# Kernel tuning notes

Hardware: AMD Instinct MI355X
Metric: run time of the kernel (lower is better)

## Reference

```python
import jax, jax.numpy as jnp
import numpy as np

B, T, D = 4, 8192, 1024
BLOCKS, TOPK, MACRO, SLOTS = 64, 16, 4, 64
RMS_EPS = 1.1920929e-07  # torch.finfo(float32).eps, F.rms_norm default


def setup_inputs() -> dict:
    key = jax.random.key(0)
    ks = jax.random.split(key, 7)
    return {
        "prev_hidden": jax.random.normal(ks[0], (B, T, D), jnp.float32),
        "prev_nll": jax.random.uniform(ks[1], (B, T), jnp.float32),
        "query": jax.random.normal(ks[2], (SLOTS, D), jnp.float32) * 0.02,
        "W_sum": jax.random.normal(ks[3], (D, 2 * D), jnp.float32) / np.sqrt(2 * D),
        "W_k": jax.random.normal(ks[4], (D, D), jnp.float32) / np.sqrt(D),
        "W_v": jax.random.normal(ks[5], (D, D), jnp.float32) / np.sqrt(D),
        "W_o": jax.random.normal(ks[6], (D, D), jnp.float32) / np.sqrt(D),
    }


def _rms_norm(x):
    return x * jax.lax.rsqrt(jnp.mean(x * x, axis=-1, keepdims=True) + RMS_EPS)


def _zscore(x):
    m = x.mean(axis=1, keepdims=True)
    s = jnp.maximum(x.std(axis=1, keepdims=True), 1e-6)  # unbiased=False
    return (x - m) / s


def reference(prev_hidden, prev_nll, query, W_sum, W_k, W_v, W_o):
    b, t, d = prev_hidden.shape
    # --- micro segments: equal blocks (t divisible by BLOCKS -> linspace edges exact)
    L = t // BLOCKS
    seg = prev_hidden.reshape(b, BLOCKS, L, d)
    seg_mean = seg.mean(axis=2)          # [B, BLOCKS, D]
    seg_last = seg[:, :, -1, :]          # [B, BLOCKS, D]
    hid_score = jnp.linalg.norm(seg_mean, axis=-1)            # [B, BLOCKS]
    sur_score = prev_nll.reshape(b, BLOCKS, L).mean(axis=-1)  # [B, BLOCKS]
    scores = _zscore(hid_score) + _zscore(sur_score)          # utility_source='both'
    idx = jnp.sort(jax.lax.top_k(scores, TOPK)[1], axis=-1)   # [B, TOPK]
    gmean = jnp.take_along_axis(seg_mean, idx[:, :, None], axis=1)
    glast = jnp.take_along_axis(seg_last, idx[:, :, None], axis=1)
    micro = jnp.concatenate([gmean, glast], axis=-1)          # [B, TOPK, 2D]
    # --- hierarchical: macro segments + global
    Lm = t // MACRO
    mseg = prev_hidden.reshape(b, MACRO, Lm, d)
    macro = jnp.concatenate([mseg.mean(axis=2), mseg[:, :, -1, :]], axis=-1)
    glob = jnp.concatenate([prev_hidden.mean(axis=1), prev_hidden[:, -1, :]], axis=-1)[:, None, :]
    feats = jnp.concatenate([micro, macro, glob], axis=1)     # [B, S=21, 2D]
    summaries = _rms_norm(jnp.einsum('bsf,df->bsd', feats, W_sum))
    # --- cross-attention of learned prefix queries over sources
    keys = jnp.einsum('bsd,ed->bse', summaries, W_k)
    vals = jnp.einsum('bsd,ed->bse', summaries, W_v)
    logits = jnp.einsum('qd,bsd->bqs', query, keys) / jnp.sqrt(jnp.float32(d))
    attn = jax.nn.softmax(logits.astype(jnp.float32), axis=-1).astype(summaries.dtype)
    prefix = jnp.einsum('bqs,bse->bqe', attn, vals)
    return jnp.einsum('bqe,oe->bqo', prefix, W_o)
```

## Files before the change

### kernel.cpp

```cpp
#include <hip/hip_runtime.h>
#include <stdint.h>
#include <stddef.h>

#define B_ 4
#define T_ 8192
#define D_ 1024
#define NBLK 64
#define SEGL 128
#define TOPK_ 16
#define NS 21
#define MPAD 96
#define RMS_EPS_ 1.1920929e-07f
#define PART 98304

typedef float f32x4 __attribute__((ext_vector_type(4)));
typedef __bf16 bf16x8 __attribute__((ext_vector_type(8)));
typedef unsigned short us8 __attribute__((ext_vector_type(8)));

__device__ __forceinline__ unsigned short f2bf(float f) {
    union { float f; unsigned int u; } v; v.f = f;
    unsigned int r = v.u + 0x7FFFu + ((v.u >> 16) & 1u);
    return (unsigned short)(r >> 16);
}
__device__ __forceinline__ float4 ld4(const float* p) { return *(const float4*)p; }

__global__ __launch_bounds__(1024) void seg_stats(
        const float* __restrict__ ph, const float* __restrict__ nll,
        float* __restrict__ seg_mean, float* __restrict__ hid, float* __restrict__ sur) {
    int g = blockIdx.x; int b = g >> 6; int blk = g & 63;
    int tid = threadIdx.x; int chunk = tid >> 8; int c = tid & 255;
    const float* base = ph + ((size_t)b * T_ + blk * SEGL + chunk * 32) * D_ + 4 * c;
    const float* p0 = base;
    const float* p1 = base + (size_t)8  * D_;
    const float* p2 = base + (size_t)16 * D_;
    const float* p3 = base + (size_t)24 * D_;
    f32x4 a0 = {0,0,0,0}, a1 = {0,0,0,0}, a2 = {0,0,0,0}, a3 = {0,0,0,0};
    #pragma unroll
    for (int r = 0; r < 8; r++) {
        float4 v0 = ld4(p0 + (size_t)r * D_);
        float4 v1 = ld4(p1 + (size_t)r * D_);
        float4 v2 = ld4(p2 + (size_t)r * D_);
        float4 v3 = ld4(p3 + (size_t)r * D_);
        a0.x += v0.x; a0.y += v0.y; a0.z += v0.z; a0.w += v0.w;
        a1.x += v1.x; a1.y += v1.y; a1.z += v1.z; a1.w += v1.w;
        a2.x += v2.x; a2.y += v2.y; a2.z += v2.z; a2.w += v2.w;
        a3.x += v3.x; a3.y += v3.y; a3.z += v3.z; a3.w += v3.w;
    }
    float sx = a0.x + a1.x + a2.x + a3.x;
    float sy = a0.y + a1.y + a2.y + a3.y;
    float sz = a0.z + a1.z + a2.z + a3.z;
    float sw = a0.w + a1.w + a2.w + a3.w;

    __shared__ float4 tmp[3][256];
    __shared__ float redw[4];
    __shared__ float surw;
    if (chunk) {
        float4 t; t.x = sx; t.y = sy; t.z = sz; t.w = sw;
        tmp[chunk - 1][c] = t;
        if (tid >= 256 && tid < 320) {
            int i = tid - 256;
            float v = nll[b * T_ + blk * SEGL + i] + nll[b * T_ + blk * SEGL + 64 + i];
            #pragma unroll
            for (int o = 32; o; o >>= 1) v += __shfl_xor(v, o);
            if (i == 0) surw = v * (1.f/128.f);
        }
    }
    __syncthreads();
    if (chunk == 0) {
        float4 t0 = tmp[0][c], t1 = tmp[1][c], t2 = tmp[2][c];
        float mx = (sx + t0.x + t1.x + t2.x) * (1.f/128.f);
        float my = (sy + t0.y + t1.y + t2.y) * (1.f/128.f);
        float mz = (sz + t0.z + t1.z + t2.z) * (1.f/128.f);
        float mw = (sw + t0.w + t1.w + t2.w) * (1.f/128.f);
        float4 m; m.x = mx; m.y = my; m.z = mz; m.w = mw;
        *(float4*)(seg_mean + (size_t)g * D_ + 4 * c) = m;
        float rv = mx*mx + my*my + mz*mz + mw*mw;
        #pragma unroll
        for (int o = 32; o; o >>= 1) rv += __shfl_xor(rv, o);
        if ((tid & 63) == 0) redw[tid >> 6] = rv;
    }
    __syncthreads();
    if (tid == 0) {
        hid[g] = sqrtf(redw[0] + redw[1] + redw[2] + redw[3]);
        sur[g] = surw;
    }
}

__global__ __launch_bounds__(256) void feats_build(
        const float* __restrict__ ph, const float* __restrict__ seg_mean,
        const float* __restrict__ hid, const float* __restrict__ sur,
        unsigned short* __restrict__ feats) {
    int r = blockIdx.x; int t = threadIdx.x;
    unsigned short* row0 = feats + (size_t)r * 2048 + 4 * t;
    unsigned short* row1 = row0 + 1024;
    if (r >= B_ * NS) {
        ushort4 z4; z4.x = z4.y = z4.z = z4.w = 0;
        *(ushort4*)row0 = z4; *(ushort4*)row1 = z4;
        return;
    }
    int b = r / NS, s = r % NS;
    __shared__ float sc[64];
    __shared__ int sidx[16];
    if (t < 64) {
        float h = hid[b * NBLK + t];
        float ss0 = sur[b * NBLK + t];
        float mh = h; for (int o = 32; o; o >>= 1) mh += __shfl_xor(mh, o); mh *= (1.f/64.f);
        float dh = h - mh; float vh = dh * dh;
        for (int o = 32; o; o >>= 1) vh += __shfl_xor(vh, o); vh *= (1.f/64.f);
        float sh = fmaxf(sqrtf(vh), 1e-6f);
        float ms = ss0; for (int o = 32; o; o >>= 1) ms += __shfl_xor(ms, o); ms *= (1.f/64.f);
        float ds = ss0 - ms; float vs = ds * ds;
        for (int o = 32; o; o >>= 1) vs += __shfl_xor(vs, o); vs *= (1.f/64.f);
        float ssd = fmaxf(sqrtf(vs), 1e-6f);
        sc[t] = dh / sh + ds / ssd;
    }
    __syncthreads();
    if (t < 64) {
        float z = sc[t];
        int rank = 0;
        for (int j = 0; j < 64; j++) {
            float oj = sc[j];
            rank += (oj > z) || (oj == z && j < t);
        }
        bool sel = rank < TOPK_;
        unsigned long long mask = __ballot(sel);
        int pos = __popcll(mask & ((1ull << t) - 1ull));
        if (sel) sidx[pos] = t;
    }
    __syncthreads();

    float mx = 0, my = 0, mz = 0, mw = 0;
    int lastrow;
    if (s < 16) {
        int blk = sidx[s];
        float4 v = ld4(seg_mean + (size_t)(b * NBLK + blk) * D_ + 4 * t);
        mx = v.x; my = v.y; mz = v.z; mw = v.w;
        lastrow = blk * SEGL + SEGL - 1;
    } else if (s < 20) {
        int m = s - 16;
        for (int j = 0; j < 16; j++) {
            float4 v = ld4(seg_mean + (size_t)(b * NBLK + m * 16 + j) * D_ + 4 * t);
            mx += v.x; my += v.y; mz += v.z; mw += v.w;
        }
        mx *= (1.f/16.f); my *= (1.f/16.f); mz *= (1.f/16.f); mw *= (1.f/16.f);
        lastrow = m * 2048 + 2047;
    } else {
        for (int j = 0; j < 64; j++) {
            float4 v = ld4(seg_mean + (size_t)(b * NBLK + j) * D_ + 4 * t);
            mx += v.x; my += v.y; mz += v.z; mw += v.w;
        }
        mx *= (1.f/64.f); my *= (1.f/64.f); mz *= (1.f/64.f); mw *= (1.f/64.f);
        lastrow = T_ - 1;
    }
    float4 lv = ld4(ph + ((size_t)b * T_ + lastrow) * D_ + 4 * t);
    ushort4 hm; hm.x = f2bf(mx); hm.y = f2bf(my); hm.z = f2bf(mz); hm.w = f2bf(mw);
    ushort4 hl; hl.x = f2bf(lv.x); hl.y = f2bf(lv.y); hl.z = f2bf(lv.z); hl.w = f2bf(lv.w);
    *(ushort4*)row0 = hm;
    *(ushort4*)row1 = hl;
}

template<int K, int AMODE, int FULLK>
__global__ __launch_bounds__(512) void gemm_lds(
        const void* __restrict__ Av,
        const float* __restrict__ B0, const float* __restrict__ B1,
        float* __restrict__ C0, float* __restrict__ C1) {
    const float* Bw = blockIdx.z ? B1 : B0;
    float* Cp       = blockIdx.z ? C1 : C0;
    int n0 = blockIdx.x * 64;
    if (!FULLK) Cp += (size_t)blockIdx.y * PART;
    int tid = threadIdx.x, wave = tid >> 6, lane = tid & 63;
    int quad = lane >> 4, l16 = lane & 15;

    __shared__ __align__(16) unsigned short Bs[64 * 264];
    __shared__ __align__(16) unsigned short As[96 * 264];

    int strip = wave >> 1, kh = wave & 1;
    f32x4 acc[6];
    #pragma unroll
    for (int i = 0; i < 6; i++) acc[i] = (f32x4){0.f, 0.f, 0.f, 0.f};
    const unsigned short* bbase = &Bs[(strip * 16 + l16) * 264 + kh * 128 + quad * 8];
    const unsigned short* abase = &As[l16 * 264 + kh * 128 + quad * 8];

    const int NCH = FULLK ? (K / 256) : 1;
    for (int ci = 0; ci < NCH; ci++) {
        int kc = FULLK ? ci : (int)blockIdx.y;
        if (ci) __syncthreads();
        #pragma unroll
        for (int i = 0; i < 4; i++) {
            int id = tid + 512 * i;
            int r = id >> 5, c = id & 31;
            const float* src = Bw + (size_t)(n0 + r) * K + kc * 256 + c * 8;
            float4 v0 = ld4(src), v1 = ld4(src + 4);
            us8 h;
            h[0] = f2bf(v0.x); h[1] = f2bf(v0.y); h[2] = f2bf(v0.z); h[3] = f2bf(v0.w);
            h[4] = f2bf(v1.x); h[5] = f2bf(v1.y); h[6] = f2bf(v1.z); h[7] = f2bf(v1.w);
            *(us8*)&Bs[r * 264 + c * 8] = h;
        }
        #pragma unroll
        for (int i = 0; i < 6; i++) {
            int id = tid + 512 * i;
            int r = id >> 5, c = id & 31;
            if (AMODE == 0) {
                const unsigned short* A = (const unsigned short*)Av;
                *(us8*)&As[r * 264 + c * 8] =
                    *(const us8*)(A + (size_t)r * K + kc * 256 + c * 8);
            } else {
                const float* A = (const float*)Av;
                const float* s0 = A + (size_t)r * K + kc * 256 + c * 8;
                float4 a0 = ld4(s0), a1 = ld4(s0 + 4);
                us8 h;
                h[0] = f2bf(a0.x); h[1] = f2bf(a0.y); h[2] = f2bf(a0.z); h[3] = f2bf(a0.w);
                h[4] = f2bf(a1.x); h[5] = f2bf(a1.y); h[6] = f2bf(a1.z); h[7] = f2bf(a1.w);
                *(us8*)&As[r * 264 + c * 8] = h;
            }
        }
        __syncthreads();
        #pragma unroll
        for (int kk = 0; kk < 128; kk += 32) {
            bf16x8 bfr = __builtin_bit_cast(bf16x8, *(const us8*)(bbase + kk));
            #pragma unroll
            for (int mi = 0; mi < 6; mi++) {
                bf16x8 af = __builtin_bit_cast(bf16x8, *(const us8*)(abase + mi * 16 * 264 + kk));
                acc[mi] = __builtin_amdgcn_mfma_f32_16x16x32_bf16(af, bfr, acc[mi], 0, 0, 0);
            }
        }
    }
    __syncthreads();

    float* scr = (float*)As;
    const int SS = 68;
    if (kh == 1) {
        #pragma unroll
        for (int mi = 0; mi < 6; mi++)
            #pragma unroll
            for (int r = 0; r < 4; r++)
                scr[(mi * 16 + quad * 4 + r) * SS + strip * 16 + l16] = acc[mi][r];
    }
    __syncthreads();
    if (kh == 0) {
        #pragma unroll
        for (int mi = 0; mi < 6; mi++)
            #pragma unroll
            for (int r = 0; r < 4; r++)
                scr[(mi * 16 + quad * 4 + r) * SS + strip * 16 + l16] += acc[mi][r];
    }
    __syncthreads();
    #pragma unroll
    for (int i = 0; i < 3; i++) {
        int id = tid + 512 * i;
        int row = id >> 4, c4 = (id & 15) << 2;
        float4 v = *(const float4*)&scr[row * SS + c4];
        *(float4*)&Cp[(size_t)row * 1024 + n0 + c4] = v;
    }
}

__global__ __launch_bounds__(256) void rmsnorm8(
        const float* __restrict__ pp, unsigned short* __restrict__ y) {
    int r = blockIdx.x; int t = threadIdx.x;
    float4 v = (float4){0.f, 0.f, 0.f, 0.f};
    #pragma unroll
    for (int c = 0; c < 8; c++) {
        float4 u = ld4(pp + (size_t)c * PART + (size_t)r * D_ + 4 * t);
        v.x += u.x; v.y += u.y; v.z += u.z; v.w += u.w;
    }
    __shared__ float red[256];
    red[t] = v.x*v.x + v.y*v.y + v.z*v.z + v.w*v.w;
    __syncthreads();
    for (int s2 = 128; s2 > 0; s2 >>= 1) { if (t < s2) red[t] += red[t + s2]; __syncthreads(); }
    float scale = rsqrtf(red[0] * (1.f/1024.f) + RMS_EPS_);
    ushort4 h;
    h.x = f2bf(v.x * scale); h.y = f2bf(v.y * scale);
    h.z = f2bf(v.z * scale); h.w = f2bf(v.w * scale);
    *(ushort4*)(y + (size_t)r * D_ + 4 * t) = h;
}

__global__ __launch_bounds__(256) void attn_out(
        const float* __restrict__ query, const float* __restrict__ keys,
        const float* __restrict__ valsO, float* __restrict__ out) {
    int g = blockIdx.x; int b = g >> 6; int q = g & 63;
    int tid = threadIdx.x, wave = tid >> 6, lane = tid & 63;
    __shared__ float attnw[24];
    const float* qrow = query + (size_t)q * D_ + lane * 16;
    float4 qv0 = ld4(qrow), qv1 = ld4(qrow + 4), qv2 = ld4(qrow + 8), qv3 = ld4(qrow + 12);
    for (int s = wave; s < NS; s += 4) {
        const float* kp = keys + (size_t)(b * NS + s) * D_ + lane * 16;
        float4 u0 = ld4(kp), u1 = ld4(kp + 4), u2 = ld4(kp + 8), u3 = ld4(kp + 12);
        float a = qv0.x*u0.x + qv0.y*u0.y + qv0.z*u0.z + qv0.w*u0.w
                + qv1.x*u1.x + qv1.y*u1.y + qv1.z*u1.z + qv1.w*u1.w
                + qv2.x*u2.x + qv2.y*u2.y + qv2.z*u2.z + qv2.w*u2.w
                + qv3.x*u3.x + qv3.y*u3.y + qv3.z*u3.z + qv3.w*u3.w;
        for (int o = 32; o; o >>= 1) a += __shfl_xor(a, o);
        if (lane == 0) attnw[s] = a * 0.03125f;
    }
    __syncthreads();
    if (tid < 32) {
        float v = (tid < NS) ? attnw[tid] : -3.0e38f;
        float m = v;
        #pragma unroll
        for (int o = 16; o; o >>= 1) m = fmaxf(m, __shfl_xor(m, o));
        float e = (tid < NS) ? expf(v - m) : 0.f;
        float s2 = e;
        #pragma unroll
        for (int o = 16; o; o >>= 1) s2 += __shfl_xor(s2, o);
        if (tid < NS) attnw[tid] = e / s2;
    }
    __syncthreads();
    float ax = 0, ay = 0, az = 0, aw = 0;
    #pragma unroll
    for (int s = 0; s < NS; s++) {
        float w = attnw[s];
        float4 v = ld4(valsO + (size_t)(b * NS + s) * D_ + 4 * tid);
        ax += w * v.x; ay += w * v.y; az += w * v.z; aw += w * v.w;
    }
    float4 o4; o4.x = ax; o4.y = ay; o4.z = az; o4.w = aw;
    *(float4*)(out + (size_t)g * D_ + 4 * tid) = o4;
}

extern "C" void kernel_launch(void* const* d_in, const int* in_sizes, int n_in,
                              void* d_out, int out_size, void* d_ws, size_t ws_size,
                              hipStream_t stream) {
    (void)in_sizes; (void)n_in; (void)out_size; (void)ws_size;
    const float* ph    = (const float*)d_in[0];
    const float* nll   = (const float*)d_in[1];
    const float* query = (const float*)d_in[2];
    const float* W_sum = (const float*)d_in[3];
    const float* W_k   = (const float*)d_in[4];
    const float* W_v   = (const float*)d_in[5];
    const float* W_o   = (const float*)d_in[6];
    float* out = (float*)d_out;

    char* ws = (char*)d_ws;
    float*          seg_mean = (float*)(ws + 0);
    float*          hid      = (float*)(ws + 1048576);
    float*          sur      = (float*)(ws + 1049600);
    unsigned short* feats    = (unsigned short*)(ws + 1050624);
    float*          presum_p = (float*)(ws + 1443840);
    unsigned short* summ_b   = (unsigned short*)(ws + 4589568);
    float*          keys     = (float*)(ws + 4786176);
    float*          vals     = (float*)(ws + 5179392);
    float*          valsO    = (float*)(ws + 5572608);

    seg_stats<<<B_ * NBLK, 1024, 0, stream>>>(ph, nll, seg_mean, hid, sur);
    feats_build<<<MPAD, 256, 0, stream>>>(ph, seg_mean, hid, sur, feats);
    gemm_lds<2048, 0, 0><<<dim3(16, 8, 1), 512, 0, stream>>>(
        feats, W_sum, nullptr, presum_p, nullptr);
    rmsnorm8<<<MPAD, 256, 0, stream>>>(presum_p, summ_b);
    gemm_lds<1024, 0, 1><<<dim3(16, 1, 2), 512, 0, stream>>>(
        summ_b, W_k, W_v, keys, vals);
    gemm_lds<1024, 2, 1><<<dim3(16, 1, 1), 512, 0, stream>>>(
        vals, W_o, nullptr, valsO, nullptr);
    attn_out<<<B_ * NBLK, 256, 0, stream>>>(query, keys, valsO, out);
}
```

Measured before the change: 260.0 us.

## Fuse post-stats pipeline into one cooperative persistent kernel with grid syncs

Six small launches (feats build, W_sum GEMM, rmsnorm, K/V GEMM, W_o GEMM, attention) are replaced by one cooperative 128-block kernel separated by grid.sync barriers. The K/V and W_o GEMMs are also split along K into partial-sum buffers that later stages reduce on load, which gives more blocks work in those phases. The aim is to remove launch gaps and raise parallelism in the GEMMs that previously ran on only 16–32 blocks. In exchange it pays grid-sync costs and redundant partial-sum reads, and it depends on cooperative launch residency.

Measured after the change: 460.7 us. 77.2% more time.

```diff
diff --git a/kernel.cpp b/kernel.cpp
--- a/kernel.cpp
+++ b/kernel.cpp
@@ -1,6 +1,9 @@
 #include <hip/hip_runtime.h>
+#include <hip/hip_cooperative_groups.h>
 #include <stdint.h>
 #include <stddef.h>
+
+namespace cg = cooperative_groups;
 
 #define B_ 4
 #define T_ 8192
@@ -86,143 +89,64 @@
     }
 }
 
-__global__ __launch_bounds__(256) void feats_build(
-        const float* __restrict__ ph, const float* __restrict__ seg_mean,
-        const float* __restrict__ hid, const float* __restrict__ sur,
-        unsigned short* __restrict__ feats) {
-    int r = blockIdx.x; int t = threadIdx.x;
-    unsigned short* row0 = feats + (size_t)r * 2048 + 4 * t;
-    unsigned short* row1 = row0 + 1024;
-    if (r >= B_ * NS) {
-        ushort4 z4; z4.x = z4.y = z4.z = z4.w = 0;
-        *(ushort4*)row0 = z4; *(ushort4*)row1 = z4;
-        return;
-    }
-    int b = r / NS, s = r % NS;
-    __shared__ float sc[64];
-    __shared__ int sidx[16];
-    if (t < 64) {
-        float h = hid[b * NBLK + t];
-        float ss0 = sur[b * NBLK + t];
-        float mh = h; for (int o = 32; o; o >>= 1) mh += __shfl_xor(mh, o); mh *= (1.f/64.f);
-        float dh = h - mh; float vh = dh * dh;
-        for (int o = 32; o; o >>= 1) vh += __shfl_xor(vh, o); vh *= (1.f/64.f);
-        float sh = fmaxf(sqrtf(vh), 1e-6f);
-        float ms = ss0; for (int o = 32; o; o >>= 1) ms += __shfl_xor(ms, o); ms *= (1.f/64.f);
-        float ds = ss0 - ms; float vs = ds * ds;
-        for (int o = 32; o; o >>= 1) vs += __shfl_xor(vs, o); vs *= (1.f/64.f);
-        float ssd = fmaxf(sqrtf(vs), 1e-6f);
-        sc[t] = dh / sh + ds / ssd;
-    }
-    __syncthreads();
-    if (t < 64) {
-        float z = sc[t];
-        int rank = 0;
-        for (int j = 0; j < 64; j++) {
-            float oj = sc[j];
-            rank += (oj > z) || (oj == z && j < t);
-        }
-        bool sel = rank < TOPK_;
-        unsigned long long mask = __ballot(sel);
-        int pos = __popcll(mask & ((1ull << t) - 1ull));
-        if (sel) sidx[pos] = t;
-    }
-    __syncthreads();
-
-    float mx = 0, my = 0, mz = 0, mw = 0;
-    int lastrow;
-    if (s < 16) {
-        int blk = sidx[s];
-        float4 v = ld4(seg_mean + (size_t)(b * NBLK + blk) * D_ + 4 * t);
-        mx = v.x; my = v.y; mz = v.z; mw = v.w;
-        lastrow = blk * SEGL + SEGL - 1;
-    } else if (s < 20) {
-        int m = s - 16;
-        for (int j = 0; j < 16; j++) {
-            float4 v = ld4(seg_mean + (size_t)(b * NBLK + m * 16 + j) * D_ + 4 * t);
-            mx += v.x; my += v.y; mz += v.z; mw += v.w;
-        }
-        mx *= (1.f/16.f); my *= (1.f/16.f); mz *= (1.f/16.f); mw *= (1.f/16.f);
-        lastrow = m * 2048 + 2047;
-    } else {
-        for (int j = 0; j < 64; j++) {
-            float4 v = ld4(seg_mean + (size_t)(b * NBLK + j) * D_ + 4 * t);
-            mx += v.x; my += v.y; mz += v.z; mw += v.w;
-        }
-        mx *= (1.f/64.f); my *= (1.f/64.f); mz *= (1.f/64.f); mw *= (1.f/64.f);
-        lastrow = T_ - 1;
-    }
-    float4 lv = ld4(ph + ((size_t)b * T_ + lastrow) * D_ + 4 * t);
-    ushort4 hm; hm.x = f2bf(mx); hm.y = f2bf(my); hm.z = f2bf(mz); hm.w = f2bf(mw);
-    ushort4 hl; hl.x = f2bf(lv.x); hl.y = f2bf(lv.y); hl.z = f2bf(lv.z); hl.w = f2bf(lv.w);
-    *(ushort4*)row0 = hm;
-    *(ushort4*)row1 = hl;
-}
-
-template<int K, int AMODE, int FULLK>
-__global__ __launch_bounds__(512) void gemm_lds(
-        const void* __restrict__ Av,
-        const float* __restrict__ B0, const float* __restrict__ B1,
-        float* __restrict__ C0, float* __restrict__ C1) {
-    const float* Bw = blockIdx.z ? B1 : B0;
-    float* Cp       = blockIdx.z ? C1 : C0;
-    int n0 = blockIdx.x * 64;
-    if (!FULLK) Cp += (size_t)blockIdx.y * PART;
-    int tid = threadIdx.x, wave = tid >> 6, lane = tid & 63;
+template<int K, int AMODE>
+__device__ __forceinline__ void gemm_chunk(
+        const void* __restrict__ Av, const float* __restrict__ Bw,
+        float* __restrict__ Cp, int n0, int kc, int tid,
+        unsigned short* Bs, unsigned short* As) {
+    int wave = tid >> 6, lane = tid & 63;
     int quad = lane >> 4, l16 = lane & 15;
-
-    __shared__ __align__(16) unsigned short Bs[64 * 264];
-    __shared__ __align__(16) unsigned short As[96 * 264];
-
     int strip = wave >> 1, kh = wave & 1;
+
+    #pragma unroll
+    for (int i = 0; i < 4; i++) {
+        int id = tid + 512 * i;
+        int r = id >> 5, c = id & 31;
+        const float* src = Bw + (size_t)(n0 + r) * K + kc * 256 + c * 8;
+        float4 v0 = ld4(src), v1 = ld4(src + 4);
+        us8 h;
+        h[0] = f2bf(v0.x); h[1] = f2bf(v0.y); h[2] = f2bf(v0.z); h[3] = f2bf(v0.w);
+        h[4] = f2bf(v1.x); h[5] = f2bf(v1.y); h[6] = f2bf(v1.z); h[7] = f2bf(v1.w);
+        *(us8*)&Bs[r * 264 + c * 8] = h;
+    }
+    #pragma unroll
+    for (int i = 0; i < 6; i++) {
+        int id = tid + 512 * i;
+        int r = id >> 5, c = id & 31;
+        if (AMODE == 0) {
+            const unsigned short* A = (const unsigned short*)Av;
+            *(us8*)&As[r * 264 + c * 8] =
+                *(const us8*)(A + (size_t)r * K + kc * 256 + c * 8);
+        } else {
+            const float* A = (const float*)Av;
+            const float* s0 = A + (size_t)r * 1024 + kc * 256 + c * 8;
+            float4 a0 = ld4(s0), a1 = ld4(s0 + 4);
+            #pragma unroll
+            for (int p = 1; p < 4; p++) {
+                float4 b0 = ld4(s0 + p * PART), b1 = ld4(s0 + p * PART + 4);
+                a0.x += b0.x; a0.y += b0.y; a0.z += b0.z; a0.w += b0.w;
+                a1.x += b1.x; a1.y += b1.y; a1.z += b1.z; a1.w += b1.w;
+            }
+            us8 h;
+            h[0] = f2bf(a0.x); h[1] = f2bf(a0.y); h[2] = f2bf(a0.z); h[3] = f2bf(a0.w);
+            h[4] = f2bf(a1.x); h[5] = f2bf(a1.y); h[6] = f2bf(a1.z); h[7] = f2bf(a1.w);
+            *(us8*)&As[r * 264 + c * 8] = h;
+        }
+    }
+    __syncthreads();
+
     f32x4 acc[6];
     #pragma unroll
     for (int i = 0; i < 6; i++) acc[i] = (f32x4){0.f, 0.f, 0.f, 0.f};
     const unsigned short* bbase = &Bs[(strip * 16 + l16) * 264 + kh * 128 + quad * 8];
     const unsigned short* abase = &As[l16 * 264 + kh * 128 + quad * 8];
-
-    const int NCH = FULLK ? (K / 256) : 1;
-    for (int ci = 0; ci < NCH; ci++) {
-        int kc = FULLK ? ci : (int)blockIdx.y;
-        if (ci) __syncthreads();
+    #pragma unroll
+    for (int kk = 0; kk < 128; kk += 32) {
+        bf16x8 bfr = __builtin_bit_cast(bf16x8, *(const us8*)(bbase + kk));
         #pragma unroll
-        for (int i = 0; i < 4; i++) {
-            int id = tid + 512 * i;
-            int r = id >> 5, c = id & 31;
-            const float* src = Bw + (size_t)(n0 + r) * K + kc * 256 + c * 8;
-            float4 v0 = ld4(src), v1 = ld4(src + 4);
-            us8 h;
-            h[0] = f2bf(v0.x); h[1] = f2bf(v0.y); h[2] = f2bf(v0.z); h[3] = f2bf(v0.w);
-            h[4] = f2bf(v1.x); h[5] = f2bf(v1.y); h[6] = f2bf(v1.z); h[7] = f2bf(v1.w);
-            *(us8*)&Bs[r * 264 + c * 8] = h;
-        }
-        #pragma unroll
-        for (int i = 0; i < 6; i++) {
-            int id = tid + 512 * i;
-            int r = id >> 5, c = id & 31;
-            if (AMODE == 0) {
-                const unsigned short* A = (const unsigned short*)Av;
-                *(us8*)&As[r * 264 + c * 8] =
-                    *(const us8*)(A + (size_t)r * K + kc * 256 + c * 8);
-            } else {
-                const float* A = (const float*)Av;
-                const float* s0 = A + (size_t)r * K + kc * 256 + c * 8;
-                float4 a0 = ld4(s0), a1 = ld4(s0 + 4);
-                us8 h;
-                h[0] = f2bf(a0.x); h[1] = f2bf(a0.y); h[2] = f2bf(a0.z); h[3] = f2bf(a0.w);
-                h[4] = f2bf(a1.x); h[5] = f2bf(a1.y); h[6] = f2bf(a1.z); h[7] = f2bf(a1.w);
-                *(us8*)&As[r * 264 + c * 8] = h;
-            }
-        }
-        __syncthreads();
-        #pragma unroll
-        for (int kk = 0; kk < 128; kk += 32) {
-            bf16x8 bfr = __builtin_bit_cast(bf16x8, *(const us8*)(bbase + kk));
-            #pragma unroll
-            for (int mi = 0; mi < 6; mi++) {
-                bf16x8 af = __builtin_bit_cast(bf16x8, *(const us8*)(abase + mi * 16 * 264 + kk));
-                acc[mi] = __builtin_amdgcn_mfma_f32_16x16x32_bf16(af, bfr, acc[mi], 0, 0, 0);
-            }
+        for (int mi = 0; mi < 6; mi++) {
+            bf16x8 af = __builtin_bit_cast(bf16x8, *(const us8*)(abase + mi * 16 * 264 + kk));
+            acc[mi] = __builtin_amdgcn_mfma_f32_16x16x32_bf16(af, bfr, acc[mi], 0, 0, 0);
         }
     }
     __syncthreads();
@@ -254,66 +178,200 @@
     }
 }
 
-__global__ __launch_bounds__(256) void rmsnorm8(
-        const float* __restrict__ pp, unsigned short* __restrict__ y) {
-    int r = blockIdx.x; int t = threadIdx.x;
-    float4 v = (float4){0.f, 0.f, 0.f, 0.f};
-    #pragma unroll
-    for (int c = 0; c < 8; c++) {
-        float4 u = ld4(pp + (size_t)c * PART + (size_t)r * D_ + 4 * t);
-        v.x += u.x; v.y += u.y; v.z += u.z; v.w += u.w;
-    }
-    __shared__ float red[256];
-    red[t] = v.x*v.x + v.y*v.y + v.z*v.z + v.w*v.w;
-    __syncthreads();
-    for (int s2 = 128; s2 > 0; s2 >>= 1) { if (t < s2) red[t] += red[t + s2]; __syncthreads(); }
-    float scale = rsqrtf(red[0] * (1.f/1024.f) + RMS_EPS_);
-    ushort4 h;
-    h.x = f2bf(v.x * scale); h.y = f2bf(v.y * scale);
-    h.z = f2bf(v.z * scale); h.w = f2bf(v.w * scale);
-    *(ushort4*)(y + (size_t)r * D_ + 4 * t) = h;
-}
-
-__global__ __launch_bounds__(256) void attn_out(
-        const float* __restrict__ query, const float* __restrict__ keys,
-        const float* __restrict__ valsO, float* __restrict__ out) {
-    int g = blockIdx.x; int b = g >> 6; int q = g & 63;
-    int tid = threadIdx.x, wave = tid >> 6, lane = tid & 63;
-    __shared__ float attnw[24];
-    const float* qrow = query + (size_t)q * D_ + lane * 16;
-    float4 qv0 = ld4(qrow), qv1 = ld4(qrow + 4), qv2 = ld4(qrow + 8), qv3 = ld4(qrow + 12);
-    for (int s = wave; s < NS; s += 4) {
-        const float* kp = keys + (size_t)(b * NS + s) * D_ + lane * 16;
-        float4 u0 = ld4(kp), u1 = ld4(kp + 4), u2 = ld4(kp + 8), u3 = ld4(kp + 12);
-        float a = qv0.x*u0.x + qv0.y*u0.y + qv0.z*u0.z + qv0.w*u0.w
-                + qv1.x*u1.x + qv1.y*u1.y + qv1.z*u1.z + qv1.w*u1.w
-                + qv2.x*u2.x + qv2.y*u2.y + qv2.z*u2.z + qv2.w*u2.w
-                + qv3.x*u3.x + qv3.y*u3.y + qv3.z*u3.z + qv3.w*u3.w;
-        for (int o = 32; o; o >>= 1) a += __shfl_xor(a, o);
-        if (lane == 0) attnw[s] = a * 0.03125f;
-    }
-    __syncthreads();
-    if (tid < 32) {
-        float v = (tid < NS) ? attnw[tid] : -3.0e38f;
-        float m = v;
+__global__ __launch_bounds__(512) void mega(
+        const float* __restrict__ ph, const float* __restrict__ query,
+        const float* __restrict__ W_sum, const float* __restrict__ W_k,
+        const float* __restrict__ W_v, const float* __restrict__ W_o,
+        const float* __restrict__ seg_mean, const float* __restrict__ hid,
+        const float* __restrict__ sur,
+        unsigned short* __restrict__ feats, float* __restrict__ presum_p,
+        unsigned short* __restrict__ summ_b,
+        float* __restrict__ keys_p, float* __restrict__ vals_p,
+        float* __restrict__ valsO_p, float* __restrict__ out) {
+    cg::grid_group grid = cg::this_grid();
+    __shared__ __align__(16) unsigned short smem_us[160 * 264];
+    unsigned short* Bs = smem_us;
+    unsigned short* As = smem_us + 64 * 264;
+    int bid = blockIdx.x, tid = threadIdx.x;
+
+    if (bid < MPAD) {
+        int r = bid, t = tid;
+        if (r >= B_ * NS) {
+            if (t < 256) {
+                ushort4 z4; z4.x = z4.y = z4.z = z4.w = 0;
+                unsigned short* row0 = feats + (size_t)r * 2048 + 4 * t;
+                *(ushort4*)row0 = z4; *(ushort4*)(row0 + 1024) = z4;
+            }
+        } else {
+            int b = r / NS, s = r % NS;
+            float* sc = (float*)smem_us;
+            int* sidx = (int*)(smem_us + 128);
+            if (t < 64) {
+                float h = hid[b * NBLK + t];
+                float ss0 = sur[b * NBLK + t];
+                float mh = h; for (int o = 32; o; o >>= 1) mh += __shfl_xor(mh, o); mh *= (1.f/64.f);
+                float dh = h - mh; float vh = dh * dh;
+                for (int o = 32; o; o >>= 1) vh += __shfl_xor(vh, o); vh *= (1.f/64.f);
+                float sh = fmaxf(sqrtf(vh), 1e-6f);
+                float ms = ss0; for (int o = 32; o; o >>= 1) ms += __shfl_xor(ms, o); ms *= (1.f/64.f);
+                float ds = ss0 - ms; float vs = ds * ds;
+                for (int o = 32; o; o >>= 1) vs += __shfl_xor(vs, o); vs *= (1.f/64.f);
+                float ssd = fmaxf(sqrtf(vs), 1e-6f);
+                sc[t] = dh / sh + ds / ssd;
+            }
+            __syncthreads();
+            if (t < 64) {
+                float z = sc[t];
+                int rank = 0;
+                for (int j = 0; j < 64; j++) {
+                    float oj = sc[j];
+                    rank += (oj > z) || (oj == z && j < t);
+                }
+                bool sel = rank < TOPK_;
+                unsigned long long mask = __ballot(sel);
+                int pos = __popcll(mask & ((1ull << t) - 1ull));
+                if (sel) sidx[pos] = t;
+            }
+            __syncthreads();
+            if (t < 256) {
+                float mx = 0, my = 0, mz = 0, mw = 0;
+                int lastrow;
+                if (s < 16) {
+                    int blk = sidx[s];
+                    float4 v = ld4(seg_mean + (size_t)(b * NBLK + blk) * D_ + 4 * t);
+                    mx = v.x; my = v.y; mz = v.z; mw = v.w;
+                    lastrow = blk * SEGL + SEGL - 1;
+                } else if (s < 20) {
+                    int m = s - 16;
+                    for (int j = 0; j < 16; j++) {
+                        float4 v = ld4(seg_mean + (size_t)(b * NBLK + m * 16 + j) * D_ + 4 * t);
+                        mx += v.x; my += v.y; mz += v.z; mw += v.w;
+                    }
+                    mx *= (1.f/16.f); my *= (1.f/16.f); mz *= (1.f/16.f); mw *= (1.f/16.f);
+                    lastrow = m * 2048 + 2047;
+                } else {
+                    for (int j = 0; j < 64; j++) {
+                        float4 v = ld4(seg_mean + (size_t)(b * NBLK + j) * D_ + 4 * t);
+                        mx += v.x; my += v.y; mz += v.z; mw += v.w;
+                    }
+                    mx *= (1.f/64.f); my *= (1.f/64.f); mz *= (1.f/64.f); mw *= (1.f/64.f);
+                    lastrow = T_ - 1;
+                }
+                float4 lv = ld4(ph + ((size_t)b * T_ + lastrow) * D_ + 4 * t);
+                ushort4 hm; hm.x = f2bf(mx); hm.y = f2bf(my); hm.z = f2bf(mz); hm.w = f2bf(mw);
+                ushort4 hl; hl.x = f2bf(lv.x); hl.y = f2bf(lv.y); hl.z = f2bf(lv.z); hl.w = f2bf(lv.w);
+                unsigned short* row0 = feats + (size_t)r * 2048 + 4 * t;
+                *(ushort4*)row0 = hm;
+                *(ushort4*)(row0 + 1024) = hl;
+            }
+        }
+    }
+    __threadfence(); grid.sync();
+
+    {
+        int strip = bid >> 3, kc = bid & 7;
+        gemm_chunk<2048, 0>(feats, W_sum, presum_p + (size_t)kc * PART,
+                            strip * 64, kc, tid, Bs, As);
+    }
+    __threadfence(); grid.sync();
+
+    if (bid < MPAD) {
+        int r = bid, t = tid;
+        float* red = (float*)smem_us;
+        float4 v = (float4){0.f, 0.f, 0.f, 0.f};
+        if (t < 256) {
+            #pragma unroll
+            for (int c = 0; c < 8; c++) {
+                float4 u = ld4(presum_p + (size_t)c * PART + (size_t)r * D_ + 4 * t);
+                v.x += u.x; v.y += u.y; v.z += u.z; v.w += u.w;
+            }
+            red[t] = v.x*v.x + v.y*v.y + v.z*v.z + v.w*v.w;
+        }
+        __syncthreads();
+        for (int s2 = 128; s2 > 0; s2 >>= 1) { if (t < s2) red[t] += red[t + s2]; __syncthreads(); }
+        float scale = rsqrtf(red[0] * (1.f/1024.f) + RMS_EPS_);
+        if (t < 256) {
+            ushort4 h;
+            h.x = f2bf(v.x * scale); h.y = f2bf(v.y * scale);
+            h.z = f2bf(v.z * scale); h.w = f2bf(v.w * scale);
+            *(ushort4*)(summ_b + (size_t)r * D_ + 4 * t) = h;
+        }
+    }
+    __threadfence(); grid.sync();
+
+    {
+        int mat = bid >> 6, inner = bid & 63;
+        int strip = inner >> 2, kc = inner & 3;
+        gemm_chunk<1024, 0>(summ_b, mat ? W_v : W_k,
+                            (mat ? vals_p : keys_p) + (size_t)kc * PART,
+                            strip * 64, kc, tid, Bs, As);
+    }
+    __threadfence(); grid.sync();
+
+    if (bid < 64) {
+        int strip = bid >> 2, kc = bid & 3;
+        gemm_chunk<1024, 1>(vals_p, W_o, valsO_p + (size_t)kc * PART,
+                            strip * 64, kc, tid, Bs, As);
+    }
+    __threadfence(); grid.sync();
+
+    {
+        int h = tid >> 8;
+        int p = bid * 2 + h;
+        int t8 = tid & 255;
+        int b = p >> 6, q = p & 63;
+        int wave4 = t8 >> 6, lane = t8 & 63;
+        float* attnw = (float*)smem_us;
+        float* aw = attnw + h * 24;
+        const float* qrow = query + (size_t)q * D_ + lane * 16;
+        float4 qv0 = ld4(qrow), qv1 = ld4(qrow + 4), qv2 = ld4(qrow + 8), qv3 = ld4(qrow + 12);
+        for (int s = wave4; s < NS; s += 4) {
+            const float* krow = keys_p + (size_t)(b * NS + s) * D_ + lane * 16;
+            float4 k0 = (float4){0,0,0,0}, k1 = k0, k2 = k0, k3 = k0;
+            #pragma unroll
+            for (int c = 0; c < 4; c++) {
+                const float* kp = krow + (size_t)c * PART;
+                float4 u0 = ld4(kp), u1 = ld4(kp + 4), u2 = ld4(kp + 8), u3 = ld4(kp + 12);
+                k0.x += u0.x; k0.y += u0.y; k0.z += u0.z; k0.w += u0.w;
+                k1.x += u1.x; k1.y += u1.y; k1.z += u1.z; k1.w += u1.w;
+                k2.x += u2.x; k2.y += u2.y; k2.z += u2.z; k2.w += u2.w;
+                k3.x += u3.x; k3.y += u3.y; k3.z += u3.z; k3.w += u3.w;
+            }
+            float a = qv0.x*k0.x + qv0.y*k0.y + qv0.z*k0.z + qv0.w*k0.w
+                    + qv1.x*k1.x + qv1.y*k1.y + qv1.z*k1.z + qv1.w*k1.w
+                    + qv2.x*k2.x + qv2.y*k2.y + qv2.z*k2.z + qv2.w*k2.w
+                    + qv3.x*k3.x + qv3.y*k3.y + qv3.z*k3.z + qv3.w*k3.w;
+            for (int o = 32; o; o >>= 1) a += __shfl_xor(a, o);
+            if (lane == 0) aw[s] = a * 0.03125f;
+        }
+        __syncthreads();
+        if (t8 < 32) {
+            float v = (t8 < NS) ? aw[t8] : -3.0e38f;
+            float m = v;
+            #pragma unroll
+            for (int o = 16; o; o >>= 1) m = fmaxf(m, __shfl_xor(m, o));
+            float e = (t8 < NS) ? expf(v - m) : 0.f;
+            float s2 = e;
+            #pragma unroll
+            for (int o = 16; o; o >>= 1) s2 += __shfl_xor(s2, o);
+            if (t8 < NS) aw[t8] = e / s2;
+        }
+        __syncthreads();
+        float ax = 0, ay = 0, az = 0, aw4 = 0;
         #pragma unroll
-        for (int o = 16; o; o >>= 1) m = fmaxf(m, __shfl_xor(m, o));
-        float e = (tid < NS) ? expf(v - m) : 0.f;
-        float s2 = e;
-        #pragma unroll
-        for (int o = 16; o; o >>= 1) s2 += __shfl_xor(s2, o);
-        if (tid < NS) attnw[tid] = e / s2;
-    }
-    __syncthreads();
-    float ax = 0, ay = 0, az = 0, aw = 0;
-    #pragma unroll
-    for (int s = 0; s < NS; s++) {
-        float w = attnw[s];
-        float4 v = ld4(valsO + (size_t)(b * NS + s) * D_ + 4 * tid);
-        ax += w * v.x; ay += w * v.y; az += w * v.z; aw += w * v.w;
-    }
-    float4 o4; o4.x = ax; o4.y = ay; o4.z = az; o4.w = aw;
-    *(float4*)(out + (size_t)g * D_ + 4 * tid) = o4;
+        for (int s = 0; s < NS; s++) {
+            float w = aw[s];
+            float4 v = (float4){0,0,0,0};
+            #pragma unroll
+            for (int c = 0; c < 4; c++) {
+                float4 u = ld4(valsO_p + (size_t)c * PART + (size_t)(b * NS + s) * D_ + 4 * t8);
+                v.x += u.x; v.y += u.y; v.z += u.z; v.w += u.w;
+            }
+            ax += w * v.x; ay += w * v.y; az += w * v.z; aw4 += w * v.w;
+        }
+        float4 o4; o4.x = ax; o4.y = ay; o4.z = az; o4.w = aw4;
+        *(float4*)(out + (size_t)p * D_ + 4 * t8) = o4;
+    }
 }
 
 extern "C" void kernel_launch(void* const* d_in, const int* in_sizes, int n_in,
@@ -336,18 +394,16 @@
     unsigned short* feats    = (unsigned short*)(ws + 1050624);
     float*          presum_p = (float*)(ws + 1443840);
     unsigned short* summ_b   = (unsigned short*)(ws + 4589568);
-    float*          keys     = (float*)(ws + 4786176);
-    float*          vals     = (float*)(ws + 5179392);
-    float*          valsO    = (float*)(ws + 5572608);
+    float*          keys_p   = (float*)(ws + 4786176);
+    float*          vals_p   = (float*)(ws + 6359040);
+    float*          valsO_p  = (float*)(ws + 7931904);
 
     seg_stats<<<B_ * NBLK, 1024, 0, stream>>>(ph, nll, seg_mean, hid, sur);
-    feats_build<<<MPAD, 256, 0, stream>>>(ph, seg_mean, hid, sur, feats);
-    gemm_lds<2048, 0, 0><<<dim3(16, 8, 1), 512, 0, stream>>>(
-        feats, W_sum, nullptr, presum_p, nullptr);
-    rmsnorm8<<<MPAD, 256, 0, stream>>>(presum_p, summ_b);
-    gemm_lds<1024, 0, 1><<<dim3(16, 1, 2), 512, 0, stream>>>(
-        summ_b, W_k, W_v, keys, vals);
-    gemm_lds<1024, 2, 1><<<dim3(16, 1, 1), 512, 0, stream>>>(
-        vals, W_o, nullptr, valsO, nullptr);
-    attn_out<<<B_ * NBLK, 256, 0, stream>>>(query, keys, valsO, out);
+
+    void* args[] = {
+        (void*)&ph, (void*)&query, (void*)&W_sum, (void*)&W_k, (void*)&W_v,
+        (void*)&W_o, (void*)&seg_mean, (void*)&hid, (void*)&sur,
+        (void*)&feats, (void*)&presum_p, (void*)&summ_b,
+        (void*)&keys_p, (void*)&vals_p, (void*)&valsO_p, (void*)&out };
+    hipLaunchCooperativeKernel((void*)mega, dim3(128), dim3(512), args, 0, stream);
 }
```

## Split K across blocks for K/V and W_o GEMMs, fusing partial reductions downstream

Applied to the files above, without the earlier changes.

The K/V and output-projection GEMMs move from a serial loop over four K chunks per block to split-K across the grid, with one 256-wide chunk per block writing partial outputs. Partial sums are reduced where they are consumed: the W_o GEMM sums the four V partials while loading A, extra blocks in that launch reduce the key partials, and attn_out sums the four valsO partials. This spreads 16-32 blocks out to 64-128 for more parallelism on a small-M problem, at the cost of extra partial-buffer traffic and redundant partial reads.

Measured after the change: 248.3 us. 4.5% less time.

```diff
diff --git a/kernel.cpp b/kernel.cpp
--- a/kernel.cpp
+++ b/kernel.cpp
@@ -159,20 +159,76 @@
     *(ushort4*)row1 = hl;
 }
 
-template<int K, int AMODE, int FULLK>
+template<int K, int AMODE, int DO_RED>
 __global__ __launch_bounds__(512) void gemm_lds(
         const void* __restrict__ Av,
         const float* __restrict__ B0, const float* __restrict__ B1,
-        float* __restrict__ C0, float* __restrict__ C1) {
+        float* __restrict__ C0, float* __restrict__ C1,
+        const float* __restrict__ R4, float* __restrict__ Rf) {
+    if (DO_RED && blockIdx.y == 4) {
+        int bx = blockIdx.x, t = threadIdx.x;
+        #pragma unroll
+        for (int i = 0; i < 3; i++) {
+            int id = t + 512 * i;
+            int rl = id >> 8, c4 = (id & 255) << 2;
+            size_t off = (size_t)(bx * 6 + rl) * 1024 + c4;
+            float4 a = ld4(R4 + off);
+            float4 b = ld4(R4 + off + PART);
+            float4 c = ld4(R4 + off + 2 * (size_t)PART);
+            float4 d = ld4(R4 + off + 3 * (size_t)PART);
+            a.x += b.x + c.x + d.x; a.y += b.y + c.y + d.y;
+            a.z += b.z + c.z + d.z; a.w += b.w + c.w + d.w;
+            *(float4*)(Rf + off) = a;
+        }
+        return;
+    }
     const float* Bw = blockIdx.z ? B1 : B0;
     float* Cp       = blockIdx.z ? C1 : C0;
     int n0 = blockIdx.x * 64;
-    if (!FULLK) Cp += (size_t)blockIdx.y * PART;
+    int kc = blockIdx.y;
+    Cp += (size_t)kc * PART;
     int tid = threadIdx.x, wave = tid >> 6, lane = tid & 63;
     int quad = lane >> 4, l16 = lane & 15;
 
     __shared__ __align__(16) unsigned short Bs[64 * 264];
     __shared__ __align__(16) unsigned short As[96 * 264];
+
+    #pragma unroll
+    for (int i = 0; i < 4; i++) {
+        int id = tid + 512 * i;
+        int r = id >> 5, c = id & 31;
+        const float* src = Bw + (size_t)(n0 + r) * K + kc * 256 + c * 8;
+        float4 v0 = ld4(src), v1 = ld4(src + 4);
+        us8 h;
+        h[0] = f2bf(v0.x); h[1] = f2bf(v0.y); h[2] = f2bf(v0.z); h[3] = f2bf(v0.w);
+        h[4] = f2bf(v1.x); h[5] = f2bf(v1.y); h[6] = f2bf(v1.z); h[7] = f2bf(v1.w);
+        *(us8*)&Bs[r * 264 + c * 8] = h;
+    }
+    #pragma unroll
+    for (int i = 0; i < 6; i++) {
+        int id = tid + 512 * i;
+        int r = id >> 5, c = id & 31;
+        if (AMODE == 0) {
+            const unsigned short* A = (const unsigned short*)Av;
+            *(us8*)&As[r * 264 + c * 8] =
+                *(const us8*)(A + (size_t)r * K + kc * 256 + c * 8);
+        } else {
+            const float* A = (const float*)Av;
+            const float* s0 = A + (size_t)r * 1024 + kc * 256 + c * 8;
+            float4 a0 = ld4(s0), a1 = ld4(s0 + 4);
+            #pragma unroll
+            for (int p = 1; p < 4; p++) {
+                float4 b0 = ld4(s0 + p * PART), b1 = ld4(s0 + p * PART + 4);
+                a0.x += b0.x; a0.y += b0.y; a0.z += b0.z; a0.w += b0.w;
+                a1.x += b1.x; a1.y += b1.y; a1.z += b1.z; a1.w += b1.w;
+            }
+            us8 h;
+            h[0] = f2bf(a0.x); h[1] = f2bf(a0.y); h[2] = f2bf(a0.z); h[3] = f2bf(a0.w);
+            h[4] = f2bf(a1.x); h[5] = f2bf(a1.y); h[6] = f2bf(a1.z); h[7] = f2bf(a1.w);
+            *(us8*)&As[r * 264 + c * 8] = h;
+        }
+    }
+    __syncthreads();
 
     int strip = wave >> 1, kh = wave & 1;
     f32x4 acc[6];
@@ -180,49 +236,13 @@
     for (int i = 0; i < 6; i++) acc[i] = (f32x4){0.f, 0.f, 0.f, 0.f};
     const unsigned short* bbase = &Bs[(strip * 16 + l16) * 264 + kh * 128 + quad * 8];
     const unsigned short* abase = &As[l16 * 264 + kh * 128 + quad * 8];
-
-    const int NCH = FULLK ? (K / 256) : 1;
-    for (int ci = 0; ci < NCH; ci++) {
-        int kc = FULLK ? ci : (int)blockIdx.y;
-        if (ci) __syncthreads();
-        #pragma unroll
-        for (int i = 0; i < 4; i++) {
-            int id = tid + 512 * i;
-            int r = id >> 5, c = id & 31;
-            const float* src = Bw + (size_t)(n0 + r) * K + kc * 256 + c * 8;
-            float4 v0 = ld4(src), v1 = ld4(src + 4);
-            us8 h;
-            h[0] = f2bf(v0.x); h[1] = f2bf(v0.y); h[2] = f2bf(v0.z); h[3] = f2bf(v0.w);
-            h[4] = f2bf(v1.x); h[5] = f2bf(v1.y); h[6] = f2bf(v1.z); h[7] = f2bf(v1.w);
-            *(us8*)&Bs[r * 264 + c * 8] = h;
-        }
-        #pragma unroll
-        for (int i = 0; i < 6; i++) {
-            int id = tid + 512 * i;
-            int r = id >> 5, c = id & 31;
-            if (AMODE == 0) {
-                const unsigned short* A = (const unsigned short*)Av;
-                *(us8*)&As[r * 264 + c * 8] =
-                    *(const us8*)(A + (size_t)r * K + kc * 256 + c * 8);
-            } else {
-                const float* A = (const float*)Av;
-                const float* s0 = A + (size_t)r * K + kc * 256 + c * 8;
-                float4 a0 = ld4(s0), a1 = ld4(s0 + 4);
-                us8 h;
-                h[0] = f2bf(a0.x); h[1] = f2bf(a0.y); h[2] = f2bf(a0.z); h[3] = f2bf(a0.w);
-                h[4] = f2bf(a1.x); h[5] = f2bf(a1.y); h[6] = f2bf(a1.z); h[7] = f2bf(a1.w);
-                *(us8*)&As[r * 264 + c * 8] = h;
-            }
-        }
-        __syncthreads();
-        #pragma unroll
-        for (int kk = 0; kk < 128; kk += 32) {
-            bf16x8 bfr = __builtin_bit_cast(bf16x8, *(const us8*)(bbase + kk));
-            #pragma unroll
-            for (int mi = 0; mi < 6; mi++) {
-                bf16x8 af = __builtin_bit_cast(bf16x8, *(const us8*)(abase + mi * 16 * 264 + kk));
-                acc[mi] = __builtin_amdgcn_mfma_f32_16x16x32_bf16(af, bfr, acc[mi], 0, 0, 0);
-            }
+    #pragma unroll
+    for (int kk = 0; kk < 128; kk += 32) {
+        bf16x8 bfr = __builtin_bit_cast(bf16x8, *(const us8*)(bbase + kk));
+        #pragma unroll
+        for (int mi = 0; mi < 6; mi++) {
+            bf16x8 af = __builtin_bit_cast(bf16x8, *(const us8*)(abase + mi * 16 * 264 + kk));
+            acc[mi] = __builtin_amdgcn_mfma_f32_16x16x32_bf16(af, bfr, acc[mi], 0, 0, 0);
         }
     }
     __syncthreads();
@@ -276,7 +296,7 @@
 
 __global__ __launch_bounds__(256) void attn_out(
         const float* __restrict__ query, const float* __restrict__ keys,
-        const float* __restrict__ valsO, float* __restrict__ out) {
+        const float* __restrict__ valsO_p, float* __restrict__ out) {
     int g = blockIdx.x; int b = g >> 6; int q = g & 63;
     int tid = threadIdx.x, wave = tid >> 6, lane = tid & 63;
     __shared__ float attnw[24];
@@ -309,7 +329,12 @@
     #pragma unroll
     for (int s = 0; s < NS; s++) {
         float w = attnw[s];
-        float4 v = ld4(valsO + (size_t)(b * NS + s) * D_ + 4 * tid);
+        float4 v = (float4){0,0,0,0};
+        #pragma unroll
+        for (int c = 0; c < 4; c++) {
+            float4 u = ld4(valsO_p + (size_t)c * PART + (size_t)(b * NS + s) * D_ + 4 * tid);
+            v.x += u.x; v.y += u.y; v.z += u.z; v.w += u.w;
+        }
         ax += w * v.x; ay += w * v.y; az += w * v.z; aw += w * v.w;
     }
     float4 o4; o4.x = ax; o4.y = ay; o4.z = az; o4.w = aw;
@@ -336,18 +361,19 @@
     unsigned short* feats    = (unsigned short*)(ws + 1050624);
     float*          presum_p = (float*)(ws + 1443840);
     unsigned short* summ_b   = (unsigned short*)(ws + 4589568);
-    float*          keys     = (float*)(ws + 4786176);
-    float*          vals     = (float*)(ws + 5179392);
-    float*          valsO    = (float*)(ws + 5572608);
+    float*          keys_p   = (float*)(ws + 4786176);
+    float*          vals_p   = (float*)(ws + 6359040);
+    float*          valsO_p  = (float*)(ws + 7931904);
+    float*          keys_f   = (float*)(ws + 9504768);
 
     seg_stats<<<B_ * NBLK, 1024, 0, stream>>>(ph, nll, seg_mean, hid, sur);
     feats_build<<<MPAD, 256, 0, stream>>>(ph, seg_mean, hid, sur, feats);
     gemm_lds<2048, 0, 0><<<dim3(16, 8, 1), 512, 0, stream>>>(
-        feats, W_sum, nullptr, presum_p, nullptr);
+        feats, W_sum, nullptr, presum_p, nullptr, nullptr, nullptr);
     rmsnorm8<<<MPAD, 256, 0, stream>>>(presum_p, summ_b);
-    gemm_lds<1024, 0, 1><<<dim3(16, 1, 2), 512, 0, stream>>>(
-        summ_b, W_k, W_v, keys, vals);
-    gemm_lds<1024, 2, 1><<<dim3(16, 1, 1), 512, 0, stream>>>(
-        vals, W_o, nullptr, valsO, nullptr);
-    attn_out<<<B_ * NBLK, 256, 0, stream>>>(query, keys, valsO, out);
-}
+    gemm_lds<1024, 0, 0><<<dim3(16, 4, 2), 512, 0, stream>>>(
+        summ_b, W_k, W_v, keys_p, vals_p, nullptr, nullptr);
+    gemm_lds<1024, 1, 1><<<dim3(16, 5, 1), 512, 0, stream>>>(
+        vals_p, W_o, nullptr, valsO_p, nullptr, keys_p, keys_f);
+    attn_out<<<B_ * NBLK, 256, 0, stream>>>(query, keys_f, valsO_p, out);
+}
```
